# Optimization experiments

Measured on AMD Instinct MI355X. Metric: run time of the kernel, lower is better.

## Reference

```python
import jax, jax.numpy as jnp
import numpy as np

D_MODEL = 1024

def setup_inputs() -> dict:
    key = jax.random.key(0)
    k1, k2, k3, k4, k5 = jax.random.split(key, 5)
    B, T, C = 8, 4096, D_MODEL
    bound = 1.0 / np.sqrt(C)
    return {
        "x": jax.random.normal(k1, (B, T, C), dtype=jnp.float32),
        "W_state": jax.random.uniform(k2, (C, C), dtype=jnp.float32, minval=-bound, maxval=bound),
        "b_state": jax.random.uniform(k3, (C,), dtype=jnp.float32, minval=-bound, maxval=bound),
        "W_gate": jax.random.uniform(k4, (C, C), dtype=jnp.float32, minval=-bound, maxval=bound),
        "b_gate": jax.random.uniform(k5, (C,), dtype=jnp.float32, minval=-bound, maxval=bound),
    }

def reference(x, W_state, b_state, W_gate, b_gate):
    # x: [B, T, C]. Precompute both projections as large batched GEMMs
    # (input-dependent parts have no time dependency), then scan the
    # tanh recurrence + sigmoid gating over T.
    B, T, C = x.shape
    px = jnp.einsum('btc,dc->btd', x, W_state) + b_state          # [B,T,C]
    g = jax.nn.sigmoid(jnp.einsum('btc,dc->btd', x, W_gate) + b_gate)  # [B,T,C]

    def step(state, inp):
        p_t, g_t = inp                    # each [B, C]
        state = jnp.tanh(p_t + state)
        return state, g_t * state

    s0 = jnp.zeros((B, C), dtype=x.dtype)
    final_state, outs = jax.lax.scan(
        step, s0, (px.transpose(1, 0, 2), g.transpose(1, 0, 2)))
    return outs.transpose(1, 0, 2), final_state  # [B,T,C], [B,C]
```

## Files before the change

### kernel.cpp

```cpp
#include <hip/hip_runtime.h>

#define DB 8
#define DT 4096
#define DC 1024
#define GM (DB*DT)
#define GN (2*DC)
#define GK DC

#define SEG 64
#define NSEG (DT/SEG)
#define WU 64
#define UCH 8

typedef _Float16 f16;
typedef _Float16 f16x8 __attribute__((ext_vector_type(8)));
typedef _Float16 f16x4 __attribute__((ext_vector_type(4)));
typedef float    f32x4 __attribute__((ext_vector_type(4)));

__device__ __forceinline__ void async_copy16(const void* g, void* l) {
    __builtin_amdgcn_global_load_lds((const __attribute__((address_space(1))) void*)g,
                                     (__attribute__((address_space(3))) void*)l,
                                     16, 0, 0);
}

__global__ __launch_bounds__(256) void conv_x_kernel(const float* __restrict__ x,
                                                     f16* __restrict__ xh) {
    const size_t i = (size_t)blockIdx.x * 256 + threadIdx.x;
    const f32x4 v = *(const f32x4*)(x + 4*i);
    f16x4 h; h.x = (f16)v.x; h.y = (f16)v.y; h.z = (f16)v.z; h.w = (f16)v.w;
    *(f16x4*)(xh + 4*i) = h;
}

__global__ __launch_bounds__(256) void conv_w_kernel(const float* __restrict__ Ws,
                                                     const float* __restrict__ Wg,
                                                     f16* __restrict__ wc) {
    const int i = blockIdx.x * 256 + threadIdx.x;
    const int e = i * 4;
    const int n = e >> 10;
    const int k = e & 1023;
    const float* src = (n < DC) ? (Ws + (size_t)n * DC + k)
                                : (Wg + (size_t)(n - DC) * DC + k);
    const f32x4 v = *(const f32x4*)src;
    f16x4 h; h.x = (f16)v.x; h.y = (f16)v.y; h.z = (f16)v.z; h.w = (f16)v.w;
    *(f16x4*)(wc + e) = h;
}

__global__ __launch_bounds__(256, 4) void gemm_kernel(
        const f16* __restrict__ xh, const f16* __restrict__ wc,
        const float* __restrict__ b_state, const float* __restrict__ b_gate,
        f16* __restrict__ pxh, f16* __restrict__ gh) {
    __shared__ f16 lds_a[128 * 64];
    __shared__ f16 lds_b[128 * 64];

    const int tid  = threadIdx.x;
    const int lane = tid & 63;
    const int xcd = blockIdx.x & 7;
    const int lin = blockIdx.x >> 3;
    const int bm  = xcd * 32 + (lin >> 4);
    const int bn  = lin & 15;
    const int wave = tid >> 6;
    const int wm   = (wave & 1) * 64;
    const int wn   = (wave >> 1) * 64;
    const int lr   = lane & 15;
    const int lq   = lane >> 4;

    f32x4 acc[4][4] = {};

    const int kc = tid & 7;
    const int rw = tid >> 3;
    const int kg = kc ^ (rw & 7);
    const int ldsbase = (tid & 192) * 16;
    const int sw = lr & 7;

    for (int kt = 0; kt < GK / 64; ++kt) {
        const int k0 = kt * 64;
        #pragma unroll
        for (int i = 0; i < 4; ++i) {
            const int row = i * 32 + rw;
            async_copy16(xh + (size_t)(bm * 128 + row) * GK + k0 + kg * 8,
                         (char*)lds_a + ldsbase + i * 4096);
            async_copy16(wc + (size_t)(bn * 128 + row) * GK + k0 + kg * 8,
                         (char*)lds_b + ldsbase + i * 4096);
        }
        __syncthreads();
        #pragma unroll
        for (int ks = 0; ks < 2; ++ks) {
            f16x8 af[4], bf[4];
            #pragma unroll
            for (int t = 0; t < 4; ++t) {
                const int pc = (ks * 4 + lq) ^ sw;
                af[t] = *(const f16x8*)&lds_a[(wm + t * 16 + lr) * 64 + pc * 8];
                bf[t] = *(const f16x8*)&lds_b[(wn + t * 16 + lr) * 64 + pc * 8];
            }
            #pragma unroll
            for (int im = 0; im < 4; ++im)
                #pragma unroll
                for (int in = 0; in < 4; ++in)
                    acc[im][in] = __builtin_amdgcn_mfma_f32_16x16x32_f16(
                        af[im], bf[in], acc[im][in], 0, 0, 0);
        }
        __syncthreads();
    }

    const int gm0 = bm * 128 + wm + lq * 4;
    const int gn0 = bn * 128 + wn + lr;
    if (bn < 8) {
        #pragma unroll
        for (int in = 0; in < 4; ++in) {
            const int gn = gn0 + in * 16;
            const float bias = b_state[gn];
            #pragma unroll
            for (int im = 0; im < 4; ++im) {
                const int gm = gm0 + im * 16;
                #pragma unroll
                for (int r = 0; r < 4; ++r)
                    pxh[(size_t)(gm + r) * DC + gn] = (f16)(acc[im][in][r] + bias);
            }
        }
    } else {
        #pragma unroll
        for (int in = 0; in < 4; ++in) {
            const int gn   = gn0 + in * 16;
            const int gcol = gn - DC;
            const float bias = b_gate[gcol];
            #pragma unroll
            for (int im = 0; im < 4; ++im) {
                const int gm = gm0 + im * 16;
                #pragma unroll
                for (int r = 0; r < 4; ++r) {
                    const float v = acc[im][in][r] + bias;
                    gh[(size_t)(gm + r) * DC + gcol] = (f16)(1.0f / (1.0f + __expf(-v)));
                }
            }
        }
    }
}

__global__ __launch_bounds__(256, 4) void scan_kernel(
        const f16* __restrict__ ph, const f16* __restrict__ gh,
        float* __restrict__ out) {
    const int tau   = blockIdx.x * 256 + threadIdx.x;
    const int seg   = tau >> 13;
    const int chain = tau & 8191;
    const size_t base = (size_t)(chain >> 10) * ((size_t)DT * DC) + (chain & 1023);
    const float L = 2.8853900817779268f;
    float sL = 0.0f, s = 0.0f;
    const int t0 = seg * SEG;

    if (seg) {
        const int tw = t0 - WU;
        f16 wA[UCH], wB[UCH];
        #pragma unroll
        for (int i = 0; i < UCH; ++i) wA[i] = ph[base + (size_t)(tw + i) * DC];
        #pragma unroll 1
        for (int ch = 0; ch < WU / UCH; ++ch) {
            #pragma unroll
            for (int i = 0; i < UCH; ++i)
                wB[i] = ph[base + (size_t)(tw + (ch + 1) * UCH + i) * DC];
            #pragma unroll
            for (int i = 0; i < UCH; ++i) {
                const float u = fmaf((float)wA[i], L, sL);
                const float e = __builtin_amdgcn_exp2f(u);
                const float r = __builtin_amdgcn_rcpf(e + 1.0f);
                sL = fmaf(-2.0f * L, r, L);
            }
            #pragma unroll
            for (int i = 0; i < UCH; ++i) wA[i] = wB[i];
        }
    }

    float pA[UCH], pB[UCH], gA[UCH], gB[UCH];
    #pragma unroll
    for (int i = 0; i < UCH; ++i) {
        const size_t idx = base + (size_t)(t0 + i) * DC;
        pA[i] = (float)ph[idx] * L;
        gA[i] = (float)gh[idx];
    }
    #pragma unroll 1
    for (int ch = 0; ch < SEG / UCH; ++ch) {
        #pragma unroll
        for (int i = 0; i < UCH; ++i) {
            const size_t idx = base + (size_t)(t0 + (ch + 1) * UCH + i) * DC;
            pB[i] = (float)ph[idx] * L;
            gB[i] = (float)gh[idx];
        }
        #pragma unroll
        for (int i = 0; i < UCH; ++i) {
            const float u = pA[i] + sL;
            const float e = __builtin_amdgcn_exp2f(u);
            const float r = __builtin_amdgcn_rcpf(e + 1.0f);
            s  = fmaf(-2.0f, r, 1.0f);
            sL = fmaf(-2.0f * L, r, L);
            out[base + (size_t)(t0 + ch * UCH + i) * DC] = gA[i] * s;
        }
        #pragma unroll
        for (int i = 0; i < UCH; ++i) { pA[i] = pB[i]; gA[i] = gB[i]; }
    }
    if (seg == NSEG - 1) out[(size_t)DB * DT * DC + chain] = s;
}

extern "C" void kernel_launch(void* const* d_in, const int* in_sizes, int n_in,
                              void* d_out, int out_size, void* d_ws, size_t ws_size,
                              hipStream_t stream) {
    const float* x  = (const float*)d_in[0];
    const float* Ws = (const float*)d_in[1];
    const float* bs = (const float*)d_in[2];
    const float* Wg = (const float*)d_in[3];
    const float* bg = (const float*)d_in[4];
    float* out = (float*)d_out;

    char* ws = (char*)d_ws;
    const size_t SZ_XH  = (size_t)GM * GK * 2;
    const size_t SZ_WC  = (size_t)GN * GK * 2;
    const size_t SZ_PXH = ((size_t)GM + 16) * DC * 2;
    f16* xh  = (f16*)ws;
    f16* wc  = (f16*)(ws + SZ_XH);
    f16* pxh = (f16*)(ws + SZ_XH + SZ_WC);
    f16* gh  = (f16*)(ws + SZ_XH + SZ_WC + SZ_PXH);

    conv_x_kernel<<<dim3(GM * GK / 1024), dim3(256), 0, stream>>>(x, xh);
    conv_w_kernel<<<dim3(GN * GK / 1024), dim3(256), 0, stream>>>(Ws, Wg, wc);
    gemm_kernel<<<dim3(4096), dim3(256), 0, stream>>>(xh, wc, bs, bg, pxh, gh);
    scan_kernel<<<dim3(DB * DC * NSEG / 256), dim3(256), 0, stream>>>(pxh, gh, out);
}
```

Measured before the change: 448.3 us.

## Rewrite GEMM as 256x256 tile, 8-wave, double-buffered ping-pong pipeline

Replaces the 128x128 single-buffered GEMM with a 256x256 block tile using 8 waves and double-buffered LDS. Global-to-LDS async copies for the next K slices are interleaved with MFMA phases, using explicit barriers, waitcnt and setprio to overlap loads with compute. The aim is to cut global traffic per FLOP and hide load latency, which the old load-sync-compute loop exposed. The cost is fiddly manual synchronisation, 128KB of LDS, a large accumulator register footprint, and fewer blocks in flight.

```diff
diff --git a/kernel.cpp b/kernel.cpp
--- a/kernel.cpp
+++ b/kernel.cpp
@@ -45,91 +45,135 @@
     *(f16x4*)(wc + e) = h;
 }
 
-__global__ __launch_bounds__(256, 4) void gemm_kernel(
+__device__ __forceinline__ void stage2(const f16* sb, f16* lb, int rowoff,
+                                       int kt, int wave) {
+    const size_t so = (size_t)rowoff * GK + (size_t)kt * 64;
+    f16* d = lb + rowoff * 64 + wave * 512;
+    async_copy16(sb + so, d);
+    async_copy16(sb + so + (size_t)64 * GK, d + 4096);
+}
+
+template<int MQ, int NQ, bool VM>
+__device__ __forceinline__ void phase(const f16* As, const f16* Bs,
+        f32x4 (&acc)[8][4], const int abase, const int bbase,
+        const int (&ksc)[2],
+        const f16* sSrc, f16* sDst, const int srow, const int kt,
+        const int wave) {
+    f16x8 af[4][2], bf[2][2];
+#pragma unroll
+    for (int t = 0; t < 4; ++t)
+#pragma unroll
+        for (int ks = 0; ks < 2; ++ks)
+            af[t][ks] = *(const f16x8*)&As[(MQ*4 + t)*2048 + abase + ksc[ks]];
+#pragma unroll
+    for (int u = 0; u < 2; ++u)
+#pragma unroll
+        for (int ks = 0; ks < 2; ++ks)
+            bf[u][ks] = *(const f16x8*)&Bs[(NQ*2 + u)*4096 + bbase + ksc[ks]];
+    stage2(sSrc, sDst, srow, kt, wave);
+    asm volatile("" ::: "memory");
+    __builtin_amdgcn_s_barrier();
+    asm volatile("s_waitcnt lgkmcnt(0)" ::: "memory");
+    __builtin_amdgcn_sched_barrier(0);
+    __builtin_amdgcn_s_setprio(1);
+#pragma unroll
+    for (int ks = 0; ks < 2; ++ks)
+#pragma unroll
+        for (int t = 0; t < 4; ++t)
+#pragma unroll
+            for (int u = 0; u < 2; ++u)
+                acc[MQ*4 + t][NQ*2 + u] = __builtin_amdgcn_mfma_f32_16x16x32_f16(
+                    af[t][ks], bf[u][ks], acc[MQ*4 + t][NQ*2 + u], 0, 0, 0);
+    __builtin_amdgcn_s_setprio(0);
+    if constexpr (VM)
+        asm volatile("s_waitcnt vmcnt(4)" ::: "memory");
+    asm volatile("" ::: "memory");
+    __builtin_amdgcn_s_barrier();
+}
+
+__global__ __launch_bounds__(512, 2) void gemm_kernel(
         const f16* __restrict__ xh, const f16* __restrict__ wc,
         const float* __restrict__ b_state, const float* __restrict__ b_gate,
         f16* __restrict__ pxh, f16* __restrict__ gh) {
-    __shared__ f16 lds_a[128 * 64];
-    __shared__ f16 lds_b[128 * 64];
+    __shared__ f16 lds_a[2][16384];
+    __shared__ f16 lds_b[2][16384];
 
     const int tid  = threadIdx.x;
     const int lane = tid & 63;
-    const int xcd = blockIdx.x & 7;
-    const int lin = blockIdx.x >> 3;
-    const int bm  = xcd * 32 + (lin >> 4);
-    const int bn  = lin & 15;
     const int wave = tid >> 6;
-    const int wm   = (wave & 1) * 64;
-    const int wn   = (wave >> 1) * 64;
-    const int lr   = lane & 15;
-    const int lq   = lane >> 4;
-
-    f32x4 acc[4][4] = {};
-
-    const int kc = tid & 7;
-    const int rw = tid >> 3;
-    const int kg = kc ^ (rw & 7);
-    const int ldsbase = (tid & 192) * 16;
-    const int sw = lr & 7;
-
-    for (int kt = 0; kt < GK / 64; ++kt) {
-        const int k0 = kt * 64;
-        #pragma unroll
-        for (int i = 0; i < 4; ++i) {
-            const int row = i * 32 + rw;
-            async_copy16(xh + (size_t)(bm * 128 + row) * GK + k0 + kg * 8,
-                         (char*)lds_a + ldsbase + i * 4096);
-            async_copy16(wc + (size_t)(bn * 128 + row) * GK + k0 + kg * 8,
-                         (char*)lds_b + ldsbase + i * 4096);
-        }
-        __syncthreads();
-        #pragma unroll
-        for (int ks = 0; ks < 2; ++ks) {
-            f16x8 af[4], bf[4];
-            #pragma unroll
-            for (int t = 0; t < 4; ++t) {
-                const int pc = (ks * 4 + lq) ^ sw;
-                af[t] = *(const f16x8*)&lds_a[(wm + t * 16 + lr) * 64 + pc * 8];
-                bf[t] = *(const f16x8*)&lds_b[(wn + t * 16 + lr) * 64 + pc * 8];
+
+    const int wg = (blockIdx.x & 7) * 128 + (blockIdx.x >> 3);
+    const int bm = wg >> 3;
+    const int bn = wg & 7;
+
+    const int lr = lane & 15, lq = lane >> 4;
+    const int wm = wave & 1,  wn = wave >> 1;
+    const int abase = (wm*16 + lr) * 64;
+    const int bbase = (wn*16 + lr) * 64;
+    const int ksc[2] = { ((0*4 + lq) ^ (lr & 7)) * 8,
+                         ((1*4 + lq) ^ (lr & 7)) * 8 };
+
+    const int rl = lane >> 3;
+    const int chs = (lane & 7) ^ rl;
+    const f16* aSrc = xh + (size_t)(bm*256 + wave*8 + rl) * GK + chs*8;
+    const f16* bSrc = wc + (size_t)(bn*256 + wave*8 + rl) * GK + chs*8;
+
+    f32x4 acc[8][4] = {};
+
+    stage2(aSrc, lds_a[0], 0,   0, wave);
+    stage2(bSrc, lds_b[0], 0,   0, wave);
+    stage2(aSrc, lds_a[0], 128, 0, wave);
+    stage2(bSrc, lds_b[0], 128, 0, wave);
+    stage2(aSrc, lds_a[1], 0,   1, wave);
+    stage2(bSrc, lds_b[1], 0,   1, wave);
+    asm volatile("s_waitcnt vmcnt(4)" ::: "memory");
+    asm volatile("" ::: "memory");
+    __builtin_amdgcn_s_barrier();
+    asm volatile("" ::: "memory");
+
+#pragma unroll 1
+    for (int j = 0; j < 8; ++j) {
+        const int k1 = 2*j + 1;
+        const int ka = (j < 7) ? 2*j + 2 : 15;
+        const int kb = (j < 7) ? 2*j + 3 : 15;
+        phase<0,0,false>(lds_a[0], lds_b[0], acc, abase, bbase, ksc, aSrc, lds_a[1], 128, k1, wave);
+        phase<0,1,false>(lds_a[0], lds_b[0], acc, abase, bbase, ksc, bSrc, lds_b[1], 128, k1, wave);
+        phase<1,0,false>(lds_a[0], lds_b[0], acc, abase, bbase, ksc, aSrc, lds_a[0], 0,   ka, wave);
+        phase<1,1,true >(lds_a[0], lds_b[0], acc, abase, bbase, ksc, bSrc, lds_b[0], 0,   ka, wave);
+        phase<0,0,false>(lds_a[1], lds_b[1], acc, abase, bbase, ksc, aSrc, lds_a[0], 128, ka, wave);
+        phase<0,1,false>(lds_a[1], lds_b[1], acc, abase, bbase, ksc, bSrc, lds_b[0], 128, ka, wave);
+        phase<1,0,false>(lds_a[1], lds_b[1], acc, abase, bbase, ksc, aSrc, lds_a[1], 0,   kb, wave);
+        phase<1,1,true >(lds_a[1], lds_b[1], acc, abase, bbase, ksc, bSrc, lds_b[1], 0,   kb, wave);
+    }
+
+    asm volatile("s_waitcnt vmcnt(0)" ::: "memory");
+
+    const int r0 = lq * 4;
+    if (bn < 4) {
+#pragma unroll
+        for (int u = 0; u < 4; ++u) {
+            const int gcol = bn*256 + (u*4 + wn)*16 + lr;
+            const float bias = b_state[gcol];
+#pragma unroll
+            for (int t = 0; t < 8; ++t) {
+                const int grow = bm*256 + (2*t + wm)*16 + r0;
+#pragma unroll
+                for (int r = 0; r < 4; ++r)
+                    pxh[(size_t)(grow + r) * DC + gcol] = (f16)(acc[t][u][r] + bias);
             }
-            #pragma unroll
-            for (int im = 0; im < 4; ++im)
-                #pragma unroll
-                for (int in = 0; in < 4; ++in)
-                    acc[im][in] = __builtin_amdgcn_mfma_f32_16x16x32_f16(
-                        af[im], bf[in], acc[im][in], 0, 0, 0);
-        }
-        __syncthreads();
-    }
-
-    const int gm0 = bm * 128 + wm + lq * 4;
-    const int gn0 = bn * 128 + wn + lr;
-    if (bn < 8) {
-        #pragma unroll
-        for (int in = 0; in < 4; ++in) {
-            const int gn = gn0 + in * 16;
-            const float bias = b_state[gn];
-            #pragma unroll
-            for (int im = 0; im < 4; ++im) {
-                const int gm = gm0 + im * 16;
-                #pragma unroll
-                for (int r = 0; r < 4; ++r)
-                    pxh[(size_t)(gm + r) * DC + gn] = (f16)(acc[im][in][r] + bias);
-            }
         }
     } else {
-        #pragma unroll
-        for (int in = 0; in < 4; ++in) {
-            const int gn   = gn0 + in * 16;
-            const int gcol = gn - DC;
+#pragma unroll
+        for (int u = 0; u < 4; ++u) {
+            const int gcol = (bn - 4)*256 + (u*4 + wn)*16 + lr;
             const float bias = b_gate[gcol];
-            #pragma unroll
-            for (int im = 0; im < 4; ++im) {
-                const int gm = gm0 + im * 16;
-                #pragma unroll
+#pragma unroll
+            for (int t = 0; t < 8; ++t) {
+                const int grow = bm*256 + (2*t + wm)*16 + r0;
+#pragma unroll
                 for (int r = 0; r < 4; ++r) {
-                    const float v = acc[im][in][r] + bias;
-                    gh[(size_t)(gm + r) * DC + gcol] = (f16)(1.0f / (1.0f + __expf(-v)));
+                    const float v = acc[t][u][r] + bias;
+                    gh[(size_t)(grow + r) * DC + gcol] = (f16)(1.0f / (1.0f + __expf(-v)));
                 }
             }
         }
@@ -220,6 +264,6 @@
 
     conv_x_kernel<<<dim3(GM * GK / 1024), dim3(256), 0, stream>>>(x, xh);
     conv_w_kernel<<<dim3(GN * GK / 1024), dim3(256), 0, stream>>>(Ws, Wg, wc);
-    gemm_kernel<<<dim3(4096), dim3(256), 0, stream>>>(xh, wc, bs, bg, pxh, gh);
+    gemm_kernel<<<dim3(1024), dim3(512), 0, stream>>>(xh, wc, bs, bg, pxh, gh);
     scan_kernel<<<dim3(DB * DC * NSEG / 256), dim3(256), 0, stream>>>(pxh, gh, out);
 }
```

After: 453.3 us. No clear change (+1.1%).
